# Optimization experiments

Measured on AMD Instinct MI355X. Metric: run time of the kernel, lower is better.

## Reference

```python
import jax, jax.numpy as jnp
import numpy as np

D = 2048      # d_model
H = 16        # n_heads
DH = D // H   # head dim = 128
L = 512       # kv_latent_dim
B = 2
S = 2048      # new tokens
PAST = 2048   # cached latent positions


def _w(key, shape, fan_in):
    return jax.random.normal(key, shape, jnp.float32) * (fan_in ** -0.5)


def setup_inputs() -> dict:
    key = jax.random.key(0)
    ks = jax.random.split(key, 8)
    return {
        "x": jax.random.normal(ks[0], (B, S, D), jnp.float32),
        "kv_cache": jax.random.normal(ks[1], (B, PAST, L), jnp.float32),
        "W_q": _w(ks[2], (D, D), D),       # nn.Linear weight [out, in]
        "W_dkv": _w(ks[3], (L, D), D),
        "W_uk": _w(ks[4], (D, L), L),
        "W_uv": _w(ks[5], (D, L), L),
        "W_o": _w(ks[6], (D, D), D),
        "ln_g": jnp.ones((L,), jnp.float32),
        "ln_b": jnp.zeros((L,), jnp.float32),
        "past_length": PAST,
    }


def _layernorm(x, g, b, eps=1e-5):
    mu = jnp.mean(x, axis=-1, keepdims=True)
    var = jnp.mean((x - mu) ** 2, axis=-1, keepdims=True)
    return (x - mu) * jax.lax.rsqrt(var + eps) * g + b


def reference(x, kv_cache, W_q, W_dkv, W_uk, W_uv, W_o, ln_g, ln_b, past_length):
    Bx, Sx, _ = x.shape
    # absorbed_k = W_q.weight @ W_uk.weight -> [D, L] -> [H, dh, L]
    absorbed = (W_q @ W_uk).reshape(H, DH, L)
    # compress to latent KV and layernorm
    new_c = _layernorm(x @ W_dkv.T, ln_g, ln_b)          # [B, S, L]
    c_kv = jnp.concatenate([kv_cache, new_c], axis=1)    # [B, T, L]
    T = c_kv.shape[1]
    # decompress V only
    v = (c_kv @ W_uv.T).reshape(Bx, T, H, DH).transpose(0, 2, 1, 3)  # [B, H, T, dh]
    # absorbed Q/K: scores_h = x_h @ absorbed_k[h] @ c_kv^T
    q = x.reshape(Bx, Sx, H, DH)                          # [B, S, H, dh]
    tmp = jnp.einsum('bshd,hdl->bhsl', q, absorbed)       # [B, H, S, L]
    scale = jnp.float32(1.0 / np.sqrt(DH))
    scores = jnp.einsum('bhsl,btl->bhst', tmp, c_kv) * scale  # [B, H, S, T]
    # causal mask: row i attends to cols j with j <= i + past_length
    mask = jnp.tril(jnp.ones((Sx, T), dtype=bool), k=past_length)
    scores = jnp.where(mask, scores, -jnp.inf)
    w = jax.nn.softmax(scores, axis=-1)
    ctx = jnp.einsum('bhst,bhtd->bshd', w, v).reshape(Bx, Sx, D)
    out = ctx @ W_o.T
    return out, c_kv
```

## Files before the change

kernel.cpp:

```cpp
#include <hip/hip_runtime.h>
#include <cstdint>

#define DV 2048
#define HH 16
#define DHD 128
#define LL 512
#define BB 2

typedef __attribute__((ext_vector_type(8))) short bf16x8;
typedef __attribute__((ext_vector_type(4))) float f32x4;
typedef __attribute__((ext_vector_type(4))) int i32x4;

typedef __attribute__((address_space(1))) const void* gas_cp;
typedef __attribute__((address_space(3))) void* las_p;

__device__ __forceinline__ void gll16(const void* g, void* l) {
    __builtin_amdgcn_global_load_lds((gas_cp)g, (las_p)l, 16, 0, 0);
}

__device__ __forceinline__ unsigned short f2b(float f) {
    union { float f; unsigned int u; } v; v.f = f;
    unsigned int u = v.u;
    return (unsigned short)((u + 0x7FFFu + ((u >> 16) & 1u)) >> 16);
}

__device__ __forceinline__ unsigned int cvt_pk_bf16(float lo, float hi) {
    unsigned int r;
    asm("v_cvt_pk_bf16_f32 %0, %1, %2" : "=v"(r) : "v"(lo), "v"(hi));
    return r;
}

#if __has_builtin(__builtin_amdgcn_exp2f)
#define EX2(x) __builtin_amdgcn_exp2f(x)
#else
#define EX2(x) exp2f(x)
#endif

__global__ void cvt_k(const float* __restrict__ in, ushort* __restrict__ out, long n) {
    long stride = (long)gridDim.x * blockDim.x * 4;
    for (long i = ((long)blockIdx.x * blockDim.x + threadIdx.x) * 4; i < n; i += stride) {
        float4 f = *(const float4*)(in + i);
        *(ushort4*)(out + i) = make_ushort4(f2b(f.x), f2b(f.y), f2b(f.z), f2b(f.w));
    }
}

__global__ void transpose_cvt_k(const float* __restrict__ in, ushort* __restrict__ outp,
                                int R, int C) {
    __shared__ float tile[64][65];
    int c0 = blockIdx.x * 64, r0 = blockIdx.y * 64;
    int tx = threadIdx.x & 63, ty = threadIdx.x >> 6;
#pragma unroll
    for (int p = 0; p < 16; ++p)
        tile[ty + p * 4][tx] = in[(long)(r0 + ty + p * 4) * C + c0 + tx];
    __syncthreads();
#pragma unroll
    for (int p = 0; p < 16; ++p)
        outp[(long)(c0 + ty + p * 4) * R + r0 + tx] = f2b(tile[tx][ty + p * 4]);
}

__global__ void kvcopy_k(const float* __restrict__ kv, float* __restrict__ cko,
                         ushort* __restrict__ ckb, int PAST, int T) {
    long n = (long)BB * PAST * LL;
    long pl2 = (long)PAST * LL;
    long stride = (long)gridDim.x * blockDim.x * 4;
    for (long i = ((long)blockIdx.x * blockDim.x + threadIdx.x) * 4; i < n; i += stride) {
        float4 f = *(const float4*)(kv + i);
        long b = i / pl2, wloc = i - b * pl2;
        long o = b * (long)T * LL + wloc;
        *(float4*)(cko + o) = f;
        *(ushort4*)(ckb + o) = make_ushort4(f2b(f.x), f2b(f.y), f2b(f.z), f2b(f.w));
    }
}

__global__ __launch_bounds__(256) void ln_k(const float* __restrict__ cpre,
                                            const float* __restrict__ g, const float* __restrict__ be,
                                            float* __restrict__ cko, ushort* __restrict__ ckb,
                                            int S, int PAST, int T) {
    int wid = threadIdx.x >> 6, lane = threadIdx.x & 63;
    int row = blockIdx.x * 4 + wid;
    int b = row / S, s = row - b * S;
    const float* xr = cpre + (long)row * LL + lane * 8;
    float4 v0 = *(const float4*)xr;
    float4 v1 = *(const float4*)(xr + 4);
    float sum = v0.x + v0.y + v0.z + v0.w + v1.x + v1.y + v1.z + v1.w;
    float sq = v0.x * v0.x + v0.y * v0.y + v0.z * v0.z + v0.w * v0.w +
               v1.x * v1.x + v1.y * v1.y + v1.z * v1.z + v1.w * v1.w;
#pragma unroll
    for (int m = 1; m < 64; m <<= 1) { sum += __shfl_xor(sum, m, 64); sq += __shfl_xor(sq, m, 64); }
    float mu = sum * (1.0f / LL);
    float var = sq * (1.0f / LL) - mu * mu;
    float rstd = rsqrtf(var + 1e-5f);
    const float* gp = g + lane * 8;
    const float* bp = be + lane * 8;
    float4 g0 = *(const float4*)gp, g1 = *(const float4*)(gp + 4);
    float4 b0 = *(const float4*)bp, b1 = *(const float4*)(bp + 4);
    float y0 = (v0.x - mu) * rstd * g0.x + b0.x;
    float y1 = (v0.y - mu) * rstd * g0.y + b0.y;
    float y2 = (v0.z - mu) * rstd * g0.z + b0.z;
    float y3 = (v0.w - mu) * rstd * g0.w + b0.w;
    float y4 = (v1.x - mu) * rstd * g1.x + b1.x;
    float y5 = (v1.y - mu) * rstd * g1.y + b1.y;
    float y6 = (v1.z - mu) * rstd * g1.z + b1.z;
    float y7 = (v1.w - mu) * rstd * g1.w + b1.w;
    long o = ((long)b * T + PAST + s) * LL + lane * 8;
    *(float4*)(cko + o) = make_float4(y0, y1, y2, y3);
    *(float4*)(cko + o + 4) = make_float4(y4, y5, y6, y7);
    *(ushort4*)(ckb + o) = make_ushort4(f2b(y0), f2b(y1), f2b(y2), f2b(y3));
    *(ushort4*)(ckb + o + 4) = make_ushort4(f2b(y4), f2b(y5), f2b(y6), f2b(y7));
}

#define G_WAIT()                                                    \
    do {                                                            \
        asm volatile("s_waitcnt vmcnt(0) lgkmcnt(0)" ::: "memory"); \
        __builtin_amdgcn_s_barrier();                               \
    } while (0)

template <bool OUT_BF16>
__global__ __launch_bounds__(256) void gemm_nt(const ushort* __restrict__ A,
                                               const ushort* __restrict__ B,
                                               void* __restrict__ Cv,
                                               int K, int lda, int ldb, int ldc,
                                               long aHi, long aLo, long bHi, long bLo,
                                               long cHi, long cLo, int zdiv, float cscale) {
    __shared__ __align__(16) ushort Asm[2][8192];
    __shared__ __align__(16) ushort Bsm[2][8192];
    const int tid = threadIdx.x, wid = tid >> 6, lane = tid & 63;
    const int z = blockIdx.z, zh = z / zdiv, zl = z % zdiv;
    A += zh * aHi + zl * aLo;
    B += zh * bHi + zl * bLo;
    const long cOff = zh * cHi + zl * cLo;
    const int m0 = blockIdx.x * 128, n0 = blockIdx.y * 128;
    const int wm = (wid >> 1) * 64, wn = (wid & 1) * 64;
    const int l15 = lane & 15;
    const int swr = (l15 & 7) << 3;
    const int vr = tid >> 3, vc = tid & 7;
    const int scol = (vc ^ (vr & 7)) << 3;
    f32x4 acc[4][4] = {};

    auto stageA = [&](int kt_, int bi) {
#pragma unroll
        for (int p = 0; p < 4; ++p)
            gll16(A + (long)(m0 + p * 32 + vr) * lda + kt_ + scol,
                  &Asm[bi][p * 2048 + tid * 8]);
    };
    auto stageB = [&](int kt_, int bi) {
#pragma unroll
        for (int p = 0; p < 4; ++p)
            gll16(B + (long)(n0 + p * 32 + vr) * ldb + kt_ + scol,
                  &Bsm[bi][p * 2048 + tid * 8]);
    };

    stageA(0, 0);
    stageB(0, 0);
    const int nkt = K >> 6;
    for (int ki = 0; ki < nkt; ++ki) {
        const int cur = ki & 1;
        G_WAIT();
        if (ki + 1 < nkt) {
            stageA((ki + 1) << 6, cur ^ 1);
            stageB((ki + 1) << 6, cur ^ 1);
        }
        __builtin_amdgcn_s_setprio(1);
#pragma unroll
        for (int kk = 0; kk < 2; ++kk) {
            const int ko = kk * 32 + ((lane >> 4) << 3);
            bf16x8 af[4], bf[4];
#pragma unroll
            for (int i = 0; i < 4; ++i)
                af[i] = *(const bf16x8*)(&Asm[cur][(wm + i * 16 + l15) * 64 + (ko ^ swr)]);
#pragma unroll
            for (int j = 0; j < 4; ++j)
                bf[j] = *(const bf16x8*)(&Bsm[cur][(wn + j * 16 + l15) * 64 + (ko ^ swr)]);
#pragma unroll
            for (int i = 0; i < 4; ++i)
#pragma unroll
                for (int j = 0; j < 4; ++j)
                    acc[i][j] = __builtin_amdgcn_mfma_f32_16x16x32_bf16(af[i], bf[j], acc[i][j], 0, 0, 0);
        }
        __builtin_amdgcn_s_setprio(0);
    }
    const int cr = (lane >> 4) * 4, cc = l15;
#pragma unroll
    for (int i = 0; i < 4; ++i) {
#pragma unroll
        for (int r = 0; r < 4; ++r) {
            const long row = m0 + wm + i * 16 + cr + r;
#pragma unroll
            for (int j = 0; j < 4; ++j) {
                const long col = n0 + wn + j * 16 + cc;
                if (OUT_BF16)
                    ((ushort*)Cv)[cOff + row * ldc + col] = f2b(acc[i][j][r] * cscale);
                else
                    ((float*)Cv)[cOff + row * ldc + col] = acc[i][j][r] * cscale;
            }
        }
    }
}

#define PH_WAIT4()                                               \
    do {                                                         \
        asm volatile("s_waitcnt vmcnt(4) lgkmcnt(0)" ::: "memory"); \
        __builtin_amdgcn_s_barrier();                            \
    } while (0)
#define PH_WAIT0()                                               \
    do {                                                         \
        asm volatile("s_waitcnt vmcnt(0) lgkmcnt(0)" ::: "memory"); \
        __builtin_amdgcn_s_barrier();                            \
    } while (0)
#define RD_BAR()                                                 \
    do {                                                         \
        asm volatile("s_waitcnt lgkmcnt(0)" ::: "memory");       \
        __builtin_amdgcn_s_barrier();                            \
    } while (0)

__global__ __launch_bounds__(256, 4) void attn_k(const ushort* __restrict__ qbf,
                                                 const ushort* __restrict__ ktb,
                                                 const ushort* __restrict__ vtb,
                                                 ushort* __restrict__ ctxb,
                                                 int S, int T, int PAST) {
    __shared__ __align__(16) ushort bufK[64 * 128];
    __shared__ __align__(16) ushort bufV[128 * 64];
    __shared__ __align__(16) ushort pl[4][16][64];
    const int tid = threadIdx.x, wid = tid >> 6, lane = tid & 63;
    const int nsb = S >> 6;
    const int nwg = BB * HH * nsb;
    const int cpx = nwg >> 3;
    const int id = (int)blockIdx.x;
    const int xcd = id & 7, k = id >> 3;
    const int r4 = k >> 5, c32 = k & 31;
    const int local = r4 * 32 + ((c32 + r4 * 8) & 31);
    const int orig = xcd * cpx + local;
    const int sblk = orig % nsb;
    const int h = (orig / nsb) % HH;
    const int b = orig / (nsb * HH);
    const int s0 = (nsb - 1 - sblk) * 64;

    const int g = lane >> 4, l15 = lane & 15, q8 = g << 3;
    const int swr = (l15 & 7) << 3;

    bf16x8 qf[4];
    {
        const ushort* qb = qbf + ((long)b * S + s0 + wid * 16 + l15) * DV + h * DHD + q8;
#pragma unroll
        for (int kk = 0; kk < 4; ++kk) qf[kk] = *(const bf16x8*)(qb + kk * 32);
    }
    f32x4 cacc[8] = {};
    f32x4 sacc[4] = {};
    float mrow = -1e30f, lrow = 0.f;
    const int rl = tid >> 4, cc16 = tid & 15;
    const int vr = tid >> 3, vc = tid & 7;
    const int nfull = (s0 + PAST) / 64;
    const ushort* kbase = ktb + (long)b * T * DV + h * DHD;
    const ushort* vbase = vtb + ((long)b * DV + h * DHD) * T;
    const int kcol = (cc16 ^ (rl & 7)) << 3;
    const int vcol = (vc ^ (vr & 7)) << 3;

    auto stageK = [&](int tt_) {
#pragma unroll
        for (int p = 0; p < 4; ++p)
            gll16(kbase + (long)(tt_ * 64 + p * 16 + rl) * DV + kcol, &bufK[p * 2048 + tid * 8]);
    };
    auto stageV = [&](int tt_) {
#pragma unroll
        for (int p = 0; p < 4; ++p)
            gll16(vbase + (long)(p * 32 + vr) * T + tt_ * 64 + vcol, &bufV[p * 2048 + tid * 8]);
    };

    stageK(0);
    stageV(0);

    for (int tt = 0; tt <= nfull; ++tt) {
        const bool last = (tt == nfull);
        PH_WAIT4();
        __builtin_amdgcn_s_setprio(1);
#pragma unroll
        for (int kk = 0; kk < 4; ++kk) {
            const int ko = kk * 32 + q8;
#pragma unroll
            for (int nf = 0; nf < 4; ++nf) {
                bf16x8 af = *(const bf16x8*)(&bufK[(nf * 16 + l15) * 128 + (ko ^ swr)]);
                sacc[nf] = __builtin_amdgcn_mfma_f32_16x16x32_bf16(af, qf[kk], sacc[nf], 0, 0, 0);
            }
        }
        __builtin_amdgcn_s_setprio(0);
        RD_BAR();
        if (!last) stageK(tt + 1);
        if (last) { PH_WAIT0(); } else { PH_WAIT4(); }
        float pm = -1e30f;
#pragma unroll
        for (int nf = 0; nf < 4; ++nf)
#pragma unroll
            for (int r = 0; r < 4; ++r) {
                float v = sacc[nf][r];
                if (last) {
                    int tl = nf * 16 + (g << 2) + r;
                    int ql = wid * 16 + l15;
                    if (tl > ql) v = -1e30f;
                }
                sacc[nf][r] = v;
                pm = fmaxf(pm, v);
            }
        pm = fmaxf(pm, __shfl_xor(pm, 16, 64));
        pm = fmaxf(pm, __shfl_xor(pm, 32, 64));
        if (__any(pm > mrow + 11.5f)) {
            float mn = fmaxf(mrow, pm);
            float al = EX2(mrow - mn);
            mrow = mn;
            lrow *= al;
#pragma unroll
            for (int r = 0; r < 4; ++r) {
                float alr = __shfl(al, (g << 2) + r, 64);
#pragma unroll
                for (int df = 0; df < 8; ++df) cacc[df][r] *= alr;
            }
        }
        float ps = 0.f;
#pragma unroll
        for (int nf = 0; nf < 4; ++nf)
#pragma unroll
            for (int r = 0; r < 4; ++r) {
                float p = EX2(sacc[nf][r] - mrow);
                sacc[nf][r] = p;
                ps += p;
            }
        ps += __shfl_xor(ps, 16, 64);
        ps += __shfl_xor(ps, 32, 64);
        lrow += ps;
#pragma unroll
        for (int nf = 0; nf < 4; ++nf)
#pragma unroll
            for (int rp = 0; rp < 2; ++rp) {
                unsigned int hb = cvt_pk_bf16(sacc[nf][rp * 2], sacc[nf][rp * 2 + 1]);
                const int tlo = nf * 16 + (g << 2) + rp * 2;
                *(unsigned int*)&pl[wid][l15][tlo ^ swr] = hb;
            }
#pragma unroll
        for (int nf = 0; nf < 4; ++nf) sacc[nf] = (f32x4){0.f, 0.f, 0.f, 0.f};
        __builtin_amdgcn_s_setprio(1);
#pragma unroll
        for (int kk = 0; kk < 2; ++kk) {
            bf16x8 a = *(const bf16x8*)(&pl[wid][l15][(kk * 32 + q8) ^ swr]);
#pragma unroll
            for (int df = 0; df < 8; ++df) {
                bf16x8 bv = *(const bf16x8*)(&bufV[(df * 16 + l15) * 64 + ((kk * 32 + q8) ^ swr)]);
                cacc[df] = __builtin_amdgcn_mfma_f32_16x16x32_bf16(a, bv, cacc[df], 0, 0, 0);
            }
        }
        __builtin_amdgcn_s_setprio(0);
        if (!last) {
            RD_BAR();
            stageV(tt + 1);
        }
    }
    const long rbase = (long)b * S + s0 + wid * 16 + (g << 2);
#pragma unroll
    for (int r = 0; r < 4; ++r) {
        float lr = __shfl(lrow, (g << 2) + r, 64);
        float inv = 1.0f / lr;
        const int d = h * DHD + l15;
#pragma unroll
        for (int df = 0; df < 8; ++df)
            ctxb[(rbase + r) * DV + d + df * 16] = f2b(cacc[df][r] * inv);
    }
}

extern "C" void kernel_launch(void* const* d_in, const int* in_sizes, int n_in,
                              void* d_out, int out_size, void* d_ws, size_t ws_size,
                              hipStream_t stream) {
    const float* x = (const float*)d_in[0];
    const float* kv = (const float*)d_in[1];
    const float* Wq = (const float*)d_in[2];
    const float* Wdkv = (const float*)d_in[3];
    const float* Wuk = (const float*)d_in[4];
    const float* Wuv = (const float*)d_in[5];
    const float* Wo = (const float*)d_in[6];
    const float* lng = (const float*)d_in[7];
    const float* lnbt = (const float*)d_in[8];
    const int S = in_sizes[0] / (BB * DV);
    const int PAST = in_sizes[1] / (BB * LL);
    const int T = S + PAST;

    float* out_p = (float*)d_out;
    float* ckv_out = out_p + (size_t)BB * S * DV;

    char* w = (char*)d_ws;
    auto take = [&](size_t bytes) { char* p = w; w += (bytes + 255) & ~(size_t)255; return p; };
    ushort* xb    = (ushort*)take((size_t)BB * S * DV * 2);
    ushort* Wqb   = (ushort*)take((size_t)DV * DV * 2);
    ushort* WukT  = (ushort*)take((size_t)DV * LL * 2);
    ushort* Wdkvb = (ushort*)take((size_t)LL * DV * 2);
    ushort* Wuvb  = (ushort*)take((size_t)DV * LL * 2);
    ushort* Wob   = (ushort*)take((size_t)DV * DV * 2);
    ushort* absb  = (ushort*)take((size_t)DV * LL * 2);
    float*  cpre  = (float*)take((size_t)BB * S * LL * 4);
    ushort* ckvb  = (ushort*)take((size_t)BB * T * LL * 2);
    ushort* vtb   = (ushort*)take((size_t)BB * DV * T * 2);
    ushort* ktb   = (ushort*)take((size_t)BB * T * DV * 2);
    ushort* ctxb  = (ushort*)take((size_t)BB * S * DV * 2);

    auto cvt = [&](const float* in, ushort* op, long n) {
        long nb = (n / 4 + 255) / 256;
        if (nb > 2048) nb = 2048;
        cvt_k<<<dim3((unsigned)nb), dim3(256), 0, stream>>>(in, op, n);
    };
    cvt(x, xb, (long)BB * S * DV);
    cvt(Wq, Wqb, (long)DV * DV);
    cvt(Wdkv, Wdkvb, (long)LL * DV);
    cvt(Wuv, Wuvb, (long)DV * LL);
    cvt(Wo, Wob, (long)DV * DV);
    transpose_cvt_k<<<dim3(LL / 64, DV / 64), dim3(256), 0, stream>>>(Wuk, WukT, DV, LL);
    kvcopy_k<<<dim3(2048), dim3(256), 0, stream>>>(kv, ckv_out, ckvb, PAST, T);

    gemm_nt<true><<<dim3(DV / 128, LL / 128, 1), dim3(256), 0, stream>>>(
        Wqb, WukT, absb, DV, DV, DV, LL, 0, 0, 0, 0, 0, 0, 1, 0.12751744900014818f);
    gemm_nt<false><<<dim3(BB * S / 128, LL / 128, 1), dim3(256), 0, stream>>>(
        xb, Wdkvb, cpre, DV, DV, DV, LL, 0, 0, 0, 0, 0, 0, 1, 1.0f);
    ln_k<<<dim3(BB * S / 4), dim3(256), 0, stream>>>(cpre, lng, lnbt, ckv_out, ckvb, S, PAST, T);
    gemm_nt<true><<<dim3(DV / 128, T / 128, BB), dim3(256), 0, stream>>>(
        Wuvb, ckvb, vtb, LL, LL, LL, T, 0, 0, (long)T * LL, 0, (long)DV * T, 0, 1, 1.0f);
    gemm_nt<true><<<dim3(T / 128, DV / 128, BB), dim3(256), 0, stream>>>(
        ckvb, absb, ktb, LL, LL, LL, DV, (long)T * LL, 0, 0, 0, (long)T * DV, 0, 1, 1.0f);
    attn_k<<<dim3(BB * HH * (S / 64)), dim3(256), 0, stream>>>(xb, ktb, vtb, ctxb, S, T, PAST);
    gemm_nt<false><<<dim3(BB * S / 128, DV / 128, 1), dim3(256), 0, stream>>>(
        ctxb, Wob, out_p, DV, DV, DV, DV, 0, 0, 0, 0, 0, 0, 1, 1.0f);
}
```

Measured before the change: 357.5 us.

## Single-buffer GEMM LDS tiles and widen K-tile swizzle in attention

The GEMM kernel drops its double-buffered LDS tiles for single A/B buffers, so each K step loads, waits on vmcnt, and then computes, with a read barrier before the next overwrite. This halves GEMM LDS use (64KB to 32KB), which may let more workgroups fit per CU, but it gives up the overlap of global loads with MFMA work inside a workgroup. Separately, the attention kernel's K-tile XOR swizzle now uses all 16 row bits instead of 8, spreading the 128-wide rows over more LDS banks to cut bank conflicts on fragment reads.

New measurement: 346.4 us. 3.1% less time.

```diff
diff --git a/kernel.cpp b/kernel.cpp
--- a/kernel.cpp
+++ b/kernel.cpp
@@ -109,7 +109,12 @@
     *(ushort4*)(ckb + o + 4) = make_ushort4(f2b(y4), f2b(y5), f2b(y6), f2b(y7));
 }
 
-#define G_WAIT()                                                    \
+#define GEMM_RD_BAR()                                               \
+    do {                                                            \
+        asm volatile("s_waitcnt lgkmcnt(0)" ::: "memory");          \
+        __builtin_amdgcn_s_barrier();                               \
+    } while (0)
+#define GEMM_VM_BAR()                                               \
     do {                                                            \
         asm volatile("s_waitcnt vmcnt(0) lgkmcnt(0)" ::: "memory"); \
         __builtin_amdgcn_s_barrier();                               \
@@ -122,8 +127,8 @@
                                                int K, int lda, int ldb, int ldc,
                                                long aHi, long aLo, long bHi, long bLo,
                                                long cHi, long cLo, int zdiv, float cscale) {
-    __shared__ __align__(16) ushort Asm[2][8192];
-    __shared__ __align__(16) ushort Bsm[2][8192];
+    __shared__ __align__(16) ushort Asm[8192];
+    __shared__ __align__(16) ushort Bsm[8192];
     const int tid = threadIdx.x, wid = tid >> 6, lane = tid & 63;
     const int z = blockIdx.z, zh = z / zdiv, zl = z % zdiv;
     A += zh * aHi + zl * aLo;
@@ -137,29 +142,23 @@
     const int scol = (vc ^ (vr & 7)) << 3;
     f32x4 acc[4][4] = {};
 
-    auto stageA = [&](int kt_, int bi) {
+    auto stageA = [&](int kt_) {
 #pragma unroll
         for (int p = 0; p < 4; ++p)
-            gll16(A + (long)(m0 + p * 32 + vr) * lda + kt_ + scol,
-                  &Asm[bi][p * 2048 + tid * 8]);
+            gll16(A + (long)(m0 + p * 32 + vr) * lda + kt_ + scol, &Asm[p * 2048 + tid * 8]);
     };
-    auto stageB = [&](int kt_, int bi) {
+    auto stageB = [&](int kt_) {
 #pragma unroll
         for (int p = 0; p < 4; ++p)
-            gll16(B + (long)(n0 + p * 32 + vr) * ldb + kt_ + scol,
-                  &Bsm[bi][p * 2048 + tid * 8]);
+            gll16(B + (long)(n0 + p * 32 + vr) * ldb + kt_ + scol, &Bsm[p * 2048 + tid * 8]);
     };
 
-    stageA(0, 0);
-    stageB(0, 0);
     const int nkt = K >> 6;
     for (int ki = 0; ki < nkt; ++ki) {
-        const int cur = ki & 1;
-        G_WAIT();
-        if (ki + 1 < nkt) {
-            stageA((ki + 1) << 6, cur ^ 1);
-            stageB((ki + 1) << 6, cur ^ 1);
-        }
+        if (ki) GEMM_RD_BAR();
+        stageA(ki << 6);
+        stageB(ki << 6);
+        GEMM_VM_BAR();
         __builtin_amdgcn_s_setprio(1);
 #pragma unroll
         for (int kk = 0; kk < 2; ++kk) {
@@ -167,10 +166,10 @@
             bf16x8 af[4], bf[4];
 #pragma unroll
             for (int i = 0; i < 4; ++i)
-                af[i] = *(const bf16x8*)(&Asm[cur][(wm + i * 16 + l15) * 64 + (ko ^ swr)]);
+                af[i] = *(const bf16x8*)(&Asm[(wm + i * 16 + l15) * 64 + (ko ^ swr)]);
 #pragma unroll
             for (int j = 0; j < 4; ++j)
-                bf[j] = *(const bf16x8*)(&Bsm[cur][(wn + j * 16 + l15) * 64 + (ko ^ swr)]);
+                bf[j] = *(const bf16x8*)(&Bsm[(wn + j * 16 + l15) * 64 + (ko ^ swr)]);
 #pragma unroll
             for (int i = 0; i < 4; ++i)
 #pragma unroll
@@ -237,6 +236,7 @@
 
     const int g = lane >> 4, l15 = lane & 15, q8 = g << 3;
     const int swr = (l15 & 7) << 3;
+    const int swrK = l15 << 3;
 
     bf16x8 qf[4];
     {
@@ -252,7 +252,7 @@
     const int nfull = (s0 + PAST) / 64;
     const ushort* kbase = ktb + (long)b * T * DV + h * DHD;
     const ushort* vbase = vtb + ((long)b * DV + h * DHD) * T;
-    const int kcol = (cc16 ^ (rl & 7)) << 3;
+    const int kcol = (cc16 ^ rl) << 3;
     const int vcol = (vc ^ (vr & 7)) << 3;
 
     auto stageK = [&](int tt_) {
@@ -278,7 +278,7 @@
             const int ko = kk * 32 + q8;
 #pragma unroll
             for (int nf = 0; nf < 4; ++nf) {
-                bf16x8 af = *(const bf16x8*)(&bufK[(nf * 16 + l15) * 128 + (ko ^ swr)]);
+                bf16x8 af = *(const bf16x8*)(&bufK[(nf * 16 + l15) * 128 + (ko ^ swrK)]);
                 sacc[nf] = __builtin_amdgcn_mfma_f32_16x16x32_bf16(af, qf[kk], sacc[nf], 0, 0, 0);
             }
         }
```
